# Kernel optimization log

Measured on AMD Instinct MI355X. Metric: run time of the kernel, lower is better.

The kernel has to match this reference:

```python
import jax, jax.numpy as jnp
import numpy as np

NUM_EMBEDDINGS = 1024
EMBEDDING_DIM = 512
SAMPLE_TOKENS = 4
CODE_DIM = EMBEDDING_DIM // SAMPLE_TOKENS  # 128
COMMITMENT_COST = 0.25


def setup_inputs() -> dict:
    key = jax.random.key(0)
    k1, k2 = jax.random.split(key)
    inputs = jax.random.normal(k1, (16, 1024, EMBEDDING_DIM), dtype=jnp.float32)
    # nn.Embedding weight init: uniform(-1/K, 1/K)
    emb_weight = jax.random.uniform(
        k2, (NUM_EMBEDDINGS, CODE_DIM), dtype=jnp.float32,
        minval=-1.0 / NUM_EMBEDDINGS, maxval=1.0 / NUM_EMBEDDINGS)
    return {"inputs": inputs, "emb_weight": emb_weight}


def reference(inputs, emb_weight):
    input_shape = inputs.shape
    flat = inputs.reshape(-1, CODE_DIM)  # [N, d]
    distances = (jnp.sum(flat * flat, axis=1, keepdims=True)
                 + jnp.sum(emb_weight * emb_weight, axis=1)
                 - 2.0 * jnp.matmul(flat, emb_weight.T))  # [N, K]
    encoding_indices = jnp.argmin(distances, axis=1)  # [N]
    # gather codebook rows instead of one-hot matmul (same math)
    quantized = jnp.take(emb_weight, encoding_indices, axis=0).reshape(input_shape)

    e_latent_loss = jnp.mean((jax.lax.stop_gradient(quantized) - inputs) ** 2)
    q_latent_loss = jnp.mean((quantized - jax.lax.stop_gradient(inputs)) ** 2)
    loss = q_latent_loss + COMMITMENT_COST * e_latent_loss

    # straight-through estimator
    quantized_ste = inputs + jax.lax.stop_gradient(quantized - inputs)

    # avg_probs = mean of one-hot encodings = code-usage histogram / N
    n = flat.shape[0]
    counts = jnp.zeros((NUM_EMBEDDINGS,), dtype=jnp.float32).at[encoding_indices].add(1.0)
    avg_probs = counts / n
    perplexity = jnp.exp(-jnp.sum(avg_probs * jnp.log(avg_probs + 1e-10)))

    return (quantized_ste, loss, perplexity)
```

## Files before the change

kernel.cpp:

```cpp
#include <hip/hip_runtime.h>
#include <cmath>

#define DIM      128
#define NELEMS   8388608
#define BAND_INT 12288
#define NBLOCKS  1024

typedef __attribute__((ext_vector_type(8))) short  short8;
typedef __attribute__((ext_vector_type(4))) float  f32x4;


__device__ inline unsigned short f2bf(float x) {
    unsigned u = __float_as_uint(x);
    unsigned r = u + 0x7FFFu + ((u >> 16) & 1u);
    return (unsigned short)(r >> 16);
}

__device__ __forceinline__ void gload_lds16(const void* g, void* l) {
    __builtin_amdgcn_global_load_lds(
        (const __attribute__((address_space(1))) void*)g,
        (__attribute__((address_space(3))) void*)l,
        16, 0, 0);
}

__global__ __launch_bounds__(256) void vq_prep_kernel(
        const float* __restrict__ e, unsigned short* __restrict__ Ehi,
        float* __restrict__ Bsq, int* __restrict__ counts, double* __restrict__ sse,
        int* __restrict__ done) {
    const int tid = threadIdx.x;
    {
        const int t  = blockIdx.x * 256 + tid;
        const int c  = t >> 4;
        const int gs = t & 15;
        const int kt = gs >> 2, qd = gs & 3;
        const int d0 = gs * 8;
        const float4 v0 = *(const float4*)(e + c * DIM + d0);
        const float4 v1 = *(const float4*)(e + c * DIM + d0 + 4);
        float f[8] = {v0.x, v0.y, v0.z, v0.w, v1.x, v1.y, v1.z, v1.w};
        unsigned short h[8];
        #pragma unroll
        for (int j = 0; j < 8; ++j) h[j] = f2bf(f[j]);
        const int ct = c >> 4, n = c & 15;
        uint4 ph;
        ph.x = h[0] | (h[1] << 16); ph.y = h[2] | (h[3] << 16);
        ph.z = h[4] | (h[5] << 16); ph.w = h[6] | (h[7] << 16);
        *(uint4*)&Ehi[(((ct * 4 + kt) * 64 + qd * 16 + n) * 8)] = ph;
    }
    {
        const int lane = tid & 31;
        #pragma unroll
        for (int r2 = 0; r2 < 2; ++r2) {
            const int row = blockIdx.x * 16 + (tid >> 5) * 2 + r2;
            const float4 xv = *(const float4*)(e + (size_t)row * DIM + lane * 4);
            float s = xv.x * xv.x + xv.y * xv.y + xv.z * xv.z + xv.w * xv.w;
            #pragma unroll
            for (int off = 16; off > 0; off >>= 1) s += __shfl_xor(s, off);
            if (lane == 0) Bsq[row] = s;
        }
    }
    if (blockIdx.x == 0) {
        ((int4*)counts)[tid] = make_int4(0, 0, 0, 0);
        if (tid == 0) { *sse = 0.0; *done = 0; }
    }
}

__global__ __launch_bounds__(256) void vq_main_kernel(
        const float* __restrict__ x, const float* __restrict__ emb,
        const unsigned short* __restrict__ Ehi, const float* __restrict__ Bsq,
        int* __restrict__ counts, double* __restrict__ sse,
        int* __restrict__ done, float* __restrict__ out) {
    __shared__ __align__(16) unsigned short Xs[8192];
    __shared__ float  sAsq[64];
    __shared__ int    sidx[64];
    __shared__ int    sIsLast;
    __shared__ double red[256];

    const int tid  = threadIdx.x;
    const int wave = tid >> 6;
    const int lane = tid & 63;
    const int n    = lane & 15;
    const int quad = lane >> 4;
    const int row0 = blockIdx.x * 64;

    {
        const int rl = tid >> 3, tq = tid & 7;
        const int dbase = tq * 16;
        const int rg_lo = rl >> 4, m = rl & 15;
        #pragma unroll
        for (int w = 0; w < 2; ++w) {
            const int r = 32 * w + rl;
            const float* xp = x + (size_t)(row0 + r) * DIM + dbase;
            float p[4];
            #pragma unroll
            for (int q = 0; q < 4; ++q) {
                const float4 v = *(const float4*)(xp + 4 * q);
                p[q] = v.x * v.x + v.y * v.y + v.z * v.z + v.w * v.w;
                const int dd = dbase + 4 * q;
                const int kt = dd >> 5, qd = (dd >> 3) & 3, j = dd & 7;
                unsigned short h0 = f2bf(v.x), h1 = f2bf(v.y), h2 = f2bf(v.z), h3 = f2bf(v.w);
                uint2 ph;
                ph.x = h0 | (h1 << 16); ph.y = h2 | (h3 << 16);
                const int rg = w * 2 + rg_lo;
                *(uint2*)&Xs[(((rg * 4 + kt) * 64 + qd * 16 + m) * 8) + j] = ph;
            }
            #pragma unroll
            for (int q = 0; q < 4; ++q) p[q] += __shfl_xor(p[q], 4);
            #pragma unroll
            for (int q = 0; q < 4; ++q) p[q] += __shfl_xor(p[q], 2);
            #pragma unroll
            for (int q = 0; q < 4; ++q) p[q] += __shfl_xor(p[q], 1);
            const float s = (p[0] + p[2]) + (p[1] + p[3]);
            if (tq == 0) sAsq[r] = s;
        }
    }
    __syncthreads();

    short8 Af[4];
    #pragma unroll
    for (int kt = 0; kt < 4; ++kt)
        Af[kt] = *(const short8*)&Xs[(((wave * 4 + kt) * 64 + lane) * 8)];
    __syncthreads();

    int K1[4], K2[4];
    #pragma unroll
    for (int i = 0; i < 4; ++i) { K1[i] = (int)0x80000000; K2[i] = (int)0x80000000; }

    const f32x4 cinit = {1.0f, 1.0f, 1.0f, 1.0f};

    #define STAGE(CUR, IT)                                                               \
        do {                                                                             \
            const char* _g = (const char*)Ehi + (size_t)(IT) * 8192 + wave * 2048 + lane * 16; \
            char*       _l = (char*)Xs + (CUR) * 8192 + wave * 2048;                     \
            gload_lds16(_g, _l);                                                         \
            gload_lds16(_g + 1024, _l + 1024);                                           \
        } while (0)

    int cur = 0;
    STAGE(0, 0);
    __syncthreads();
    for (int it = 0; it < 32; ++it) {
        if (it < 31) STAGE(cur ^ 1, it + 1);
        #pragma unroll
        for (int c = 0; c < 2; ++c) {
            const int ct = 2 * it + c;
            short8 Bf[4];
            #pragma unroll
            for (int kt = 0; kt < 4; ++kt)
                Bf[kt] = *(const short8*)&Xs[(size_t)cur * 4096 + c * 2048 + (kt * 64 + lane) * 8];
            f32x4 a = cinit;
            #pragma unroll
            for (int kt = 0; kt < 4; ++kt)
                a = __builtin_amdgcn_mfma_f32_16x16x32_bf16(Af[kt], Bf[kt], a, 0, 0, 0);
            #pragma unroll
            for (int r = 0; r < 4; ++r) {
                const int k0 = (__float_as_int(a[r]) & (int)0xFFFFFFC0) | ct;
                const int t0 = min(K1[r], k0);
                K1[r] = max(K1[r], k0);
                K2[r] = max(K2[r], t0);
            }
        }
        __syncthreads();
        cur ^= 1;
    }
    #undef STAGE

    int2* sc = (int2*)Xs;
    #pragma unroll
    for (int r = 0; r < 4; ++r) {
        const int lr = wave * 16 + quad * 4 + r;
        sc[lr * 17 + n] = make_int2(K1[r], K2[r]);
    }
    __syncthreads();

    if (tid < 64) {
        const int row  = tid;
        const int rowg = row0 + row;
        const int2* ent = (const int2*)sc + row * 17;
        int mx = (int)0x80000000;
        #pragma unroll
        for (int e2 = 0; e2 < 16; ++e2) mx = max(mx, ent[e2].x);
        const int thr = mx - BAND_INT;
        int ck[8];
        int nc = 0;
        #pragma unroll
        for (int e2 = 0; e2 < 16; ++e2) {
            const int2 kk = ent[e2];
            if (kk.x >= thr && nc < 8) ck[nc++] = ((kk.x & 63) << 4) | e2;
            if (kk.y >= thr && nc < 8) ck[nc++] = ((kk.y & 63) << 4) | e2;
        }
        float bd = INFINITY;
        int   bk = 0x7fffffff;
        const float4* xr = (const float4*)(x + (size_t)rowg * DIM);
        const float   aq = sAsq[row];
        for (int c = 0; c < nc; ++c) {
            const int k = ck[c];
            const float4* er = (const float4*)(emb + (size_t)k * DIM);
            float acc = 0.0f;
            #pragma unroll 4
            for (int dd = 0; dd < 32; ++dd) {
                const float4 xv = xr[dd];
                const float4 ev = er[dd];
                acc += xv.x * ev.x;
                acc += xv.y * ev.y;
                acc += xv.z * ev.z;
                acc += xv.w * ev.w;
            }
            const float t    = aq + Bsq[k];
            const float dist = t - 2.0f * acc;
            if (dist < bd || (dist == bd && k < bk)) { bd = dist; bk = k; }
        }
        sidx[row] = bk;
        atomicAdd(&counts[bk], 1);
        float ss = bd;
        #pragma unroll
        for (int off = 32; off > 0; off >>= 1) ss += __shfl_down(ss, off);
        if (tid == 0) atomicAdd(sse, (double)ss);
    }
    __syncthreads();

    #pragma unroll
    for (int i = tid; i < 2048; i += 256) {
        const int row = i >> 5, d4 = i & 31;
        const int k = sidx[row];
        const float4 xv = *((const float4*)(x + (size_t)(row0 + row) * DIM) + d4);
        const float4 qv = *((const float4*)emb + (size_t)k * 32 + d4);
        float4 ov;
        ov.x = xv.x + (qv.x - xv.x);
        ov.y = xv.y + (qv.y - xv.y);
        ov.z = xv.z + (qv.z - xv.z);
        ov.w = xv.w + (qv.w - xv.w);
        *((float4*)out + (size_t)(row0 + row) * 32 + d4) = ov;
    }

    if (tid == 0) sIsLast = (atomicAdd(done, 1) == NBLOCKS - 1);
    __syncthreads();
    if (sIsLast) {
        __threadfence();
        double s = 0.0;
        #pragma unroll
        for (int k = tid; k < 1024; k += 256) {
            const float p = (float)counts[k] * (1.0f / 65536.0f);
            s += (double)p * log((double)p + 1e-10);
        }
        red[tid] = s;
        __syncthreads();
        for (int st = 128; st > 0; st >>= 1) {
            if (tid < st) red[tid] += red[tid + st];
            __syncthreads();
        }
        if (tid == 0) {
            const float m = (float)(*sse * (1.0 / 8388608.0));
            out[NELEMS]     = m + 0.25f * m;
            out[NELEMS + 1] = (float)exp(-red[0]);
        }
    }
}

extern "C" void kernel_launch(void* const* d_in, const int* in_sizes, int n_in,
                              void* d_out, int out_size, void* d_ws, size_t ws_size,
                              hipStream_t stream) {
    const float* x   = (const float*)d_in[0];
    const float* emb = (const float*)d_in[1];
    float* out = (float*)d_out;

    char*           ws     = (char*)d_ws;
    float*          Bsq    = (float*)(ws + 0);
    int*            counts = (int*)(ws + 4096);
    double*         sse    = (double*)(ws + 8192);
    int*            done   = (int*)(ws + 12288);
    unsigned short* Ehi    = (unsigned short*)(ws + 16384);

    vq_prep_kernel<<<64, 256, 0, stream>>>(emb, Ehi, Bsq, counts, sse, done);
    vq_main_kernel<<<NBLOCKS, 256, 0, stream>>>(x, emb, Ehi, Bsq, counts, sse, done, out);
}
```

Before: 145.7 us.

## Split main kernel into scan and separate STE/finalize kernel

Moves the straight-through output write and the final loss/perplexity reduction out of the main kernel into a third launch. Nearest-code indices now go through a global buffer instead of shared memory. This drops the last-block done counter and its fence, which lets the scan kernel use fewer resources and run without a tail. In exchange it adds an extra launch and re-reads x from global memory, which is 32 MB of extra traffic.

Measured after the change: 152.7 us. 4.8% more time.

```diff
diff --git a/kernel.cpp b/kernel.cpp
--- a/kernel.cpp
+++ b/kernel.cpp
@@ -4,7 +4,6 @@
 #define DIM      128
 #define NELEMS   8388608
 #define BAND_INT 12288
-#define NBLOCKS  1024
 
 typedef __attribute__((ext_vector_type(8))) short  short8;
 typedef __attribute__((ext_vector_type(4))) float  f32x4;
@@ -25,8 +24,7 @@
 
 __global__ __launch_bounds__(256) void vq_prep_kernel(
         const float* __restrict__ e, unsigned short* __restrict__ Ehi,
-        float* __restrict__ Bsq, int* __restrict__ counts, double* __restrict__ sse,
-        int* __restrict__ done) {
+        float* __restrict__ Bsq, int* __restrict__ counts, double* __restrict__ sse) {
     const int tid = threadIdx.x;
     {
         const int t  = blockIdx.x * 256 + tid;
@@ -60,20 +58,17 @@
     }
     if (blockIdx.x == 0) {
         ((int4*)counts)[tid] = make_int4(0, 0, 0, 0);
-        if (tid == 0) { *sse = 0.0; *done = 0; }
-    }
-}
-
-__global__ __launch_bounds__(256) void vq_main_kernel(
+        if (tid == 0) *sse = 0.0;
+    }
+}
+
+__global__ __launch_bounds__(256) void vq_scan_kernel(
         const float* __restrict__ x, const float* __restrict__ emb,
         const unsigned short* __restrict__ Ehi, const float* __restrict__ Bsq,
         int* __restrict__ counts, double* __restrict__ sse,
-        int* __restrict__ done, float* __restrict__ out) {
+        int* __restrict__ sidx_g) {
     __shared__ __align__(16) unsigned short Xs[8192];
     __shared__ float  sAsq[64];
-    __shared__ int    sidx[64];
-    __shared__ int    sIsLast;
-    __shared__ double red[256];
 
     const int tid  = threadIdx.x;
     const int wave = tid >> 6;
@@ -209,50 +204,51 @@
             const float dist = t - 2.0f * acc;
             if (dist < bd || (dist == bd && k < bk)) { bd = dist; bk = k; }
         }
-        sidx[row] = bk;
+        sidx_g[rowg] = bk;
         atomicAdd(&counts[bk], 1);
         float ss = bd;
         #pragma unroll
         for (int off = 32; off > 0; off >>= 1) ss += __shfl_down(ss, off);
         if (tid == 0) atomicAdd(sse, (double)ss);
     }
-    __syncthreads();
-
-    #pragma unroll
-    for (int i = tid; i < 2048; i += 256) {
-        const int row = i >> 5, d4 = i & 31;
-        const int k = sidx[row];
-        const float4 xv = *((const float4*)(x + (size_t)(row0 + row) * DIM) + d4);
+}
+
+__global__ __launch_bounds__(256) void vq_ste_kernel(
+        const float* __restrict__ x, const float* __restrict__ emb,
+        const int* __restrict__ sidx, const int* __restrict__ counts,
+        const double* __restrict__ sse, float* __restrict__ out) {
+    const int tid = threadIdx.x;
+
+    if (blockIdx.x == 0 && tid < 64) {
+        double s = 0.0;
+        #pragma unroll
+        for (int k = tid; k < 1024; k += 64) {
+            const float p = (float)counts[k] * (1.0f / 65536.0f);
+            s += (double)p * log((double)p + 1e-10);
+        }
+        #pragma unroll
+        for (int off = 32; off > 0; off >>= 1) s += __shfl_down(s, off);
+        if (tid == 0) {
+            const float m = (float)(*sse * (1.0 / 8388608.0));
+            out[NELEMS]     = m + 0.25f * m;
+            out[NELEMS + 1] = (float)exp(-s);
+        }
+    }
+
+    const int total  = NELEMS / 4;
+    const int stride = gridDim.x * 256;
+    for (int i = blockIdx.x * 256 + tid; i < total; i += stride) {
+        const int row = i >> 5;
+        const int d4  = i & 31;
+        const int k   = sidx[row];
+        const float4 xv = *((const float4*)x + (size_t)row * 32 + d4);
         const float4 qv = *((const float4*)emb + (size_t)k * 32 + d4);
         float4 ov;
         ov.x = xv.x + (qv.x - xv.x);
         ov.y = xv.y + (qv.y - xv.y);
         ov.z = xv.z + (qv.z - xv.z);
         ov.w = xv.w + (qv.w - xv.w);
-        *((float4*)out + (size_t)(row0 + row) * 32 + d4) = ov;
-    }
-
-    if (tid == 0) sIsLast = (atomicAdd(done, 1) == NBLOCKS - 1);
-    __syncthreads();
-    if (sIsLast) {
-        __threadfence();
-        double s = 0.0;
-        #pragma unroll
-        for (int k = tid; k < 1024; k += 256) {
-            const float p = (float)counts[k] * (1.0f / 65536.0f);
-            s += (double)p * log((double)p + 1e-10);
-        }
-        red[tid] = s;
-        __syncthreads();
-        for (int st = 128; st > 0; st >>= 1) {
-            if (tid < st) red[tid] += red[tid + st];
-            __syncthreads();
-        }
-        if (tid == 0) {
-            const float m = (float)(*sse * (1.0 / 8388608.0));
-            out[NELEMS]     = m + 0.25f * m;
-            out[NELEMS + 1] = (float)exp(-red[0]);
-        }
+        *((float4*)out + i) = ov;
     }
 }
 
@@ -267,9 +263,10 @@
     float*          Bsq    = (float*)(ws + 0);
     int*            counts = (int*)(ws + 4096);
     double*         sse    = (double*)(ws + 8192);
-    int*            done   = (int*)(ws + 12288);
     unsigned short* Ehi    = (unsigned short*)(ws + 16384);
-
-    vq_prep_kernel<<<64, 256, 0, stream>>>(emb, Ehi, Bsq, counts, sse, done);
-    vq_main_kernel<<<NBLOCKS, 256, 0, stream>>>(x, emb, Ehi, Bsq, counts, sse, done, out);
-}
+    int*            sidx   = (int*)(ws + 278528);
+
+    vq_prep_kernel<<<64, 256, 0, stream>>>(emb, Ehi, Bsq, counts, sse);
+    vq_scan_kernel<<<1024, 256, 0, stream>>>(x, emb, Ehi, Bsq, counts, sse, sidx);
+    vq_ste_kernel<<<2048, 256, 0, stream>>>(x, emb, sidx, counts, sse, out);
+}
```

## Triple-buffer codebook staging and split waves into 2x2 row/column tiles

Applied to the files above, without the earlier changes.

Codebook tiles are now staged through three LDS buffers instead of two. Each iteration waits only for the older load with an explicit vmcnt wait and a raw s_barrier, so loads run two tiles ahead of compute. Waves are remapped so each owns two 16-row A tiles and one of the two 16-column B tiles per stage, which halves B-fragment LDS reads per MFMA and doubles the per-lane top-2 state. The candidate merge now scans 32 partial entries per row instead of 16. In exchange it uses more LDS and registers, and relies on hand-written wait counts being correct.

Result: slower. 174.3 us (+19.7%).

```diff
diff --git a/kernel.cpp b/kernel.cpp
--- a/kernel.cpp
+++ b/kernel.cpp
@@ -69,7 +69,7 @@
         const unsigned short* __restrict__ Ehi, const float* __restrict__ Bsq,
         int* __restrict__ counts, double* __restrict__ sse,
         int* __restrict__ done, float* __restrict__ out) {
-    __shared__ __align__(16) unsigned short Xs[8192];
+    __shared__ __align__(16) unsigned short Xs[12288];
     __shared__ float  sAsq[64];
     __shared__ int    sidx[64];
     __shared__ int    sIsLast;
@@ -80,6 +80,8 @@
     const int lane = tid & 63;
     const int n    = lane & 15;
     const int quad = lane >> 4;
+    const int wa   = wave >> 1;
+    const int ctb  = wave & 1;
     const int row0 = blockIdx.x * 64;
 
     {
@@ -115,78 +117,105 @@
     }
     __syncthreads();
 
-    short8 Af[4];
+    short8 Af[2][4];
     #pragma unroll
-    for (int kt = 0; kt < 4; ++kt)
-        Af[kt] = *(const short8*)&Xs[(((wave * 4 + kt) * 64 + lane) * 8)];
-    __syncthreads();
-
-    int K1[4], K2[4];
+    for (int rti = 0; rti < 2; ++rti)
+        #pragma unroll
+        for (int kt = 0; kt < 4; ++kt)
+            Af[rti][kt] = *(const short8*)&Xs[((((wa * 2 + rti) * 4 + kt) * 64 + lane) * 8)];
+    __syncthreads();
+
+    int K1[8], K2[8];
     #pragma unroll
-    for (int i = 0; i < 4; ++i) { K1[i] = (int)0x80000000; K2[i] = (int)0x80000000; }
+    for (int i = 0; i < 8; ++i) { K1[i] = (int)0x80000000; K2[i] = (int)0x80000000; }
 
     const f32x4 cinit = {1.0f, 1.0f, 1.0f, 1.0f};
 
-    #define STAGE(CUR, IT)                                                               \
+    #define STAGE(BUF, IT)                                                               \
         do {                                                                             \
             const char* _g = (const char*)Ehi + (size_t)(IT) * 8192 + wave * 2048 + lane * 16; \
-            char*       _l = (char*)Xs + (CUR) * 8192 + wave * 2048;                     \
+            char*       _l = (char*)Xs + (size_t)(BUF) * 8192 + wave * 2048;             \
             gload_lds16(_g, _l);                                                         \
             gload_lds16(_g + 1024, _l + 1024);                                           \
         } while (0)
 
-    int cur = 0;
+    #define COMPUTETILE(BUF, IT)                                                         \
+        do {                                                                             \
+            const int _ct = 2 * (IT) + ctb;                                              \
+            short8 Bf[4];                                                                \
+            _Pragma("unroll")                                                            \
+            for (int _kt = 0; _kt < 4; ++_kt)                                            \
+                Bf[_kt] = *(const short8*)&Xs[(size_t)(BUF) * 4096 + ctb * 2048 + (_kt * 64 + lane) * 8]; \
+            f32x4 _a0 = cinit, _a1 = cinit;                                              \
+            _Pragma("unroll")                                                            \
+            for (int _kt = 0; _kt < 4; ++_kt) {                                          \
+                _a0 = __builtin_amdgcn_mfma_f32_16x16x32_bf16(Af[0][_kt], Bf[_kt], _a0, 0, 0, 0); \
+                _a1 = __builtin_amdgcn_mfma_f32_16x16x32_bf16(Af[1][_kt], Bf[_kt], _a1, 0, 0, 0); \
+            }                                                                            \
+            _Pragma("unroll")                                                            \
+            for (int _r = 0; _r < 4; ++_r) {                                             \
+                int _k = (__float_as_int(_a0[_r]) & (int)0xFFFFFFC0) | _ct;              \
+                int _t = min(K1[_r], _k);                                                \
+                K1[_r] = max(K1[_r], _k);                                                \
+                K2[_r] = max(K2[_r], _t);                                                \
+                _k = (__float_as_int(_a1[_r]) & (int)0xFFFFFFC0) | _ct;                  \
+                _t = min(K1[4 + _r], _k);                                                \
+                K1[4 + _r] = max(K1[4 + _r], _k);                                        \
+                K2[4 + _r] = max(K2[4 + _r], _t);                                        \
+            }                                                                            \
+        } while (0)
+
+    int cur = 0, nxt = 1, fut = 2;
     STAGE(0, 0);
-    __syncthreads();
-    for (int it = 0; it < 32; ++it) {
-        if (it < 31) STAGE(cur ^ 1, it + 1);
-        #pragma unroll
-        for (int c = 0; c < 2; ++c) {
-            const int ct = 2 * it + c;
-            short8 Bf[4];
-            #pragma unroll
-            for (int kt = 0; kt < 4; ++kt)
-                Bf[kt] = *(const short8*)&Xs[(size_t)cur * 4096 + c * 2048 + (kt * 64 + lane) * 8];
-            f32x4 a = cinit;
-            #pragma unroll
-            for (int kt = 0; kt < 4; ++kt)
-                a = __builtin_amdgcn_mfma_f32_16x16x32_bf16(Af[kt], Bf[kt], a, 0, 0, 0);
-            #pragma unroll
-            for (int r = 0; r < 4; ++r) {
-                const int k0 = (__float_as_int(a[r]) & (int)0xFFFFFFC0) | ct;
-                const int t0 = min(K1[r], k0);
-                K1[r] = max(K1[r], k0);
-                K2[r] = max(K2[r], t0);
-            }
-        }
-        __syncthreads();
-        cur ^= 1;
-    }
+    STAGE(1, 1);
+    asm volatile("s_waitcnt vmcnt(2)" ::: "memory");
+    __builtin_amdgcn_sched_barrier(0);
+    __builtin_amdgcn_s_barrier();
+    __builtin_amdgcn_sched_barrier(0);
+
+    for (int it = 0; it < 30; ++it) {
+        STAGE(fut, it + 2);
+        COMPUTETILE(cur, it);
+        asm volatile("s_waitcnt vmcnt(2)" ::: "memory");
+        __builtin_amdgcn_sched_barrier(0);
+        __builtin_amdgcn_s_barrier();
+        __builtin_amdgcn_sched_barrier(0);
+        const int tmp = cur; cur = nxt; nxt = fut; fut = tmp;
+    }
+    COMPUTETILE(cur, 30);
+    __syncthreads();
+    { const int tmp = cur; cur = nxt; nxt = fut; fut = tmp; }
+    COMPUTETILE(cur, 31);
+    __syncthreads();
     #undef STAGE
+    #undef COMPUTETILE
 
     int2* sc = (int2*)Xs;
     #pragma unroll
-    for (int r = 0; r < 4; ++r) {
-        const int lr = wave * 16 + quad * 4 + r;
-        sc[lr * 17 + n] = make_int2(K1[r], K2[r]);
-    }
+    for (int rti = 0; rti < 2; ++rti)
+        #pragma unroll
+        for (int r = 0; r < 4; ++r) {
+            const int lr = (wa * 2 + rti) * 16 + quad * 4 + r;
+            sc[lr * 33 + ctb * 16 + n] = make_int2(K1[rti * 4 + r], K2[rti * 4 + r]);
+        }
     __syncthreads();
 
     if (tid < 64) {
         const int row  = tid;
         const int rowg = row0 + row;
-        const int2* ent = (const int2*)sc + row * 17;
+        const int2* ent = (const int2*)sc + row * 33;
         int mx = (int)0x80000000;
         #pragma unroll
-        for (int e2 = 0; e2 < 16; ++e2) mx = max(mx, ent[e2].x);
+        for (int e2 = 0; e2 < 32; ++e2) mx = max(mx, ent[e2].x);
         const int thr = mx - BAND_INT;
         int ck[8];
         int nc = 0;
         #pragma unroll
-        for (int e2 = 0; e2 < 16; ++e2) {
+        for (int e2 = 0; e2 < 32; ++e2) {
             const int2 kk = ent[e2];
-            if (kk.x >= thr && nc < 8) ck[nc++] = ((kk.x & 63) << 4) | e2;
-            if (kk.y >= thr && nc < 8) ck[nc++] = ((kk.y & 63) << 4) | e2;
+            const int ne = e2 & 15;
+            if (kk.x >= thr && nc < 8) ck[nc++] = ((kk.x & 63) << 4) | ne;
+            if (kk.y >= thr && nc < 8) ck[nc++] = ((kk.y & 63) << 4) | ne;
         }
         float bd = INFINITY;
         int   bk = 0x7fffffff;
```

## Use single-wave blocks over 32 rows with barrier-free double-buffered codebook streaming

Applied to the files above, without the earlier changes.

Each block becomes one 64-thread wave handling 32 rows (two MFMA row tiles that share each B fragment), and the grid doubles. Codebook tiles are loaded straight into LDS with an s_waitcnt-based two-deep pipeline instead of __syncthreads per iteration. The top-2 tracking uses v_med3, and the reductions switch to wave shuffles. The aim is to cut barrier overhead and reuse each B load across two row tiles. The cost is that each wave now streams the whole codebook into LDS by itself, with more LDS traffic per row, and correctness relies on the hand-written vmcnt counts.

After: 161.8 us. 11.1% more time.

```diff
diff --git a/kernel.cpp b/kernel.cpp
--- a/kernel.cpp
+++ b/kernel.cpp
@@ -4,7 +4,7 @@
 #define DIM      128
 #define NELEMS   8388608
 #define BAND_INT 12288
-#define NBLOCKS  1024
+#define NBLOCKS  2048
 
 typedef __attribute__((ext_vector_type(8))) short  short8;
 typedef __attribute__((ext_vector_type(4))) float  f32x4;
@@ -64,31 +64,29 @@
     }
 }
 
-__global__ __launch_bounds__(256) void vq_main_kernel(
+__global__ __launch_bounds__(64) void vq_main_kernel(
         const float* __restrict__ x, const float* __restrict__ emb,
         const unsigned short* __restrict__ Ehi, const float* __restrict__ Bsq,
         int* __restrict__ counts, double* __restrict__ sse,
         int* __restrict__ done, float* __restrict__ out) {
     __shared__ __align__(16) unsigned short Xs[8192];
-    __shared__ float  sAsq[64];
-    __shared__ int    sidx[64];
+    __shared__ float  sAsq[32];
+    __shared__ int    sidx[32];
     __shared__ int    sIsLast;
-    __shared__ double red[256];
 
     const int tid  = threadIdx.x;
-    const int wave = tid >> 6;
-    const int lane = tid & 63;
+    const int lane = tid;
     const int n    = lane & 15;
     const int quad = lane >> 4;
-    const int row0 = blockIdx.x * 64;
+    const int row0 = blockIdx.x * 32;
 
     {
         const int rl = tid >> 3, tq = tid & 7;
         const int dbase = tq * 16;
-        const int rg_lo = rl >> 4, m = rl & 15;
-        #pragma unroll
-        for (int w = 0; w < 2; ++w) {
-            const int r = 32 * w + rl;
+        #pragma unroll
+        for (int w = 0; w < 4; ++w) {
+            const int r = 8 * w + rl;
+            const int rg = r >> 4, m = r & 15;
             const float* xp = x + (size_t)(row0 + r) * DIM + dbase;
             float p[4];
             #pragma unroll
@@ -100,7 +98,6 @@
                 unsigned short h0 = f2bf(v.x), h1 = f2bf(v.y), h2 = f2bf(v.z), h3 = f2bf(v.w);
                 uint2 ph;
                 ph.x = h0 | (h1 << 16); ph.y = h2 | (h3 << 16);
-                const int rg = w * 2 + rg_lo;
                 *(uint2*)&Xs[(((rg * 4 + kt) * 64 + qd * 16 + m) * 8) + j] = ph;
             }
             #pragma unroll
@@ -115,64 +112,86 @@
     }
     __syncthreads();
 
-    short8 Af[4];
-    #pragma unroll
-    for (int kt = 0; kt < 4; ++kt)
-        Af[kt] = *(const short8*)&Xs[(((wave * 4 + kt) * 64 + lane) * 8)];
-    __syncthreads();
-
-    int K1[4], K2[4];
-    #pragma unroll
-    for (int i = 0; i < 4; ++i) { K1[i] = (int)0x80000000; K2[i] = (int)0x80000000; }
+    short8 Af[2][4];
+    #pragma unroll
+    for (int rti = 0; rti < 2; ++rti)
+        #pragma unroll
+        for (int kt = 0; kt < 4; ++kt)
+            Af[rti][kt] = *(const short8*)&Xs[(((rti * 4 + kt) * 64 + lane) * 8)];
+    __syncthreads();
+
+    int K1[8], K2[8];
+    #pragma unroll
+    for (int i = 0; i < 8; ++i) { K1[i] = (int)0x80000000; K2[i] = (int)0x80000000; }
 
     const f32x4 cinit = {1.0f, 1.0f, 1.0f, 1.0f};
 
-    #define STAGE(CUR, IT)                                                               \
-        do {                                                                             \
-            const char* _g = (const char*)Ehi + (size_t)(IT) * 8192 + wave * 2048 + lane * 16; \
-            char*       _l = (char*)Xs + (CUR) * 8192 + wave * 2048;                     \
-            gload_lds16(_g, _l);                                                         \
-            gload_lds16(_g + 1024, _l + 1024);                                           \
+    #define STAGE(BUF, IT)                                                         \
+        do {                                                                       \
+            const char* _g = (const char*)Ehi + (size_t)(IT) * 8192 + lane * 16;   \
+            char*       _l = (char*)Xs + (size_t)(BUF) * 8192 + lane * 16;         \
+            _Pragma("unroll")                                                      \
+            for (int _k = 0; _k < 8; ++_k)                                         \
+                gload_lds16(_g + _k * 1024, _l + _k * 1024);                       \
         } while (0)
 
-    int cur = 0;
+    #define COMPUTETILE(BUF, IT)                                                   \
+        do {                                                                       \
+            _Pragma("unroll")                                                      \
+            for (int _c = 0; _c < 2; ++_c) {                                       \
+                const int _ct = 2 * (IT) + _c;                                     \
+                short8 Bf[4];                                                      \
+                _Pragma("unroll")                                                  \
+                for (int _kt = 0; _kt < 4; ++_kt)                                  \
+                    Bf[_kt] = *(const short8*)&Xs[(size_t)(BUF) * 4096 + _c * 2048 + (_kt * 64 + lane) * 8]; \
+                f32x4 _a0 = cinit, _a1 = cinit;                                    \
+                _Pragma("unroll")                                                  \
+                for (int _kt = 0; _kt < 4; ++_kt) {                                \
+                    _a0 = __builtin_amdgcn_mfma_f32_16x16x32_bf16(Af[0][_kt], Bf[_kt], _a0, 0, 0, 0); \
+                    _a1 = __builtin_amdgcn_mfma_f32_16x16x32_bf16(Af[1][_kt], Bf[_kt], _a1, 0, 0, 0); \
+                }                                                                  \
+                _Pragma("unroll")                                                  \
+                for (int _r = 0; _r < 4; ++_r) {                                   \
+                    int _k0 = (__float_as_int(_a0[_r]) & (int)0xFFFFFFC0) | _ct;   \
+                    int _k2n;   \
+                    asm("v_med3_i32 %0, %1, %2, %3"                                \
+                        : "=v"(_k2n) : "v"(K1[_r]), "v"(K2[_r]), "v"(_k0));        \
+                    K2[_r] = _k2n;                                                 \
+                    K1[_r] = max(K1[_r], _k0);                                     \
+                    int _k1 = (__float_as_int(_a1[_r]) & (int)0xFFFFFFC0) | _ct;   \
+                    asm("v_med3_i32 %0, %1, %2, %3"                                \
+                        : "=v"(_k2n) : "v"(K1[4 + _r]), "v"(K2[4 + _r]), "v"(_k1)); \
+                    K2[4 + _r] = _k2n;                                             \
+                    K1[4 + _r] = max(K1[4 + _r], _k1);                             \
+                }                                                                  \
+            }                                                                      \
+        } while (0)
+
     STAGE(0, 0);
-    __syncthreads();
-    for (int it = 0; it < 32; ++it) {
-        if (it < 31) STAGE(cur ^ 1, it + 1);
-        #pragma unroll
-        for (int c = 0; c < 2; ++c) {
-            const int ct = 2 * it + c;
-            short8 Bf[4];
-            #pragma unroll
-            for (int kt = 0; kt < 4; ++kt)
-                Bf[kt] = *(const short8*)&Xs[(size_t)cur * 4096 + c * 2048 + (kt * 64 + lane) * 8];
-            f32x4 a = cinit;
-            #pragma unroll
-            for (int kt = 0; kt < 4; ++kt)
-                a = __builtin_amdgcn_mfma_f32_16x16x32_bf16(Af[kt], Bf[kt], a, 0, 0, 0);
-            #pragma unroll
-            for (int r = 0; r < 4; ++r) {
-                const int k0 = (__float_as_int(a[r]) & (int)0xFFFFFFC0) | ct;
-                const int t0 = min(K1[r], k0);
-                K1[r] = max(K1[r], k0);
-                K2[r] = max(K2[r], t0);
-            }
-        }
-        __syncthreads();
-        cur ^= 1;
-    }
+    STAGE(1, 1);
+    for (int it = 0; it < 31; ++it) {
+        asm volatile("s_waitcnt vmcnt(8)" ::: "memory");
+        COMPUTETILE(it & 1, it);
+        if (it < 30) STAGE(it & 1, it + 2);
+    }
+    asm volatile("s_waitcnt vmcnt(0)" ::: "memory");
+    COMPUTETILE(1, 31);
+    __syncthreads();
     #undef STAGE
+    #undef COMPUTETILE
 
     int2* sc = (int2*)Xs;
     #pragma unroll
-    for (int r = 0; r < 4; ++r) {
-        const int lr = wave * 16 + quad * 4 + r;
-        sc[lr * 17 + n] = make_int2(K1[r], K2[r]);
-    }
-    __syncthreads();
-
-    if (tid < 64) {
+    for (int rti = 0; rti < 2; ++rti)
+        #pragma unroll
+        for (int r = 0; r < 4; ++r) {
+            const int lr = rti * 16 + quad * 4 + r;
+            sc[lr * 17 + n] = make_int2(K1[rti * 4 + r], K2[rti * 4 + r]);
+        }
+    __syncthreads();
+
+    float ssum = 0.0f;
+    if (tid < 32) {
         const int row  = tid;
         const int rowg = row0 + row;
         const int2* ent = (const int2*)sc + row * 17;
@@ -211,15 +230,15 @@
         }
         sidx[row] = bk;
         atomicAdd(&counts[bk], 1);
-        float ss = bd;
-        #pragma unroll
-        for (int off = 32; off > 0; off >>= 1) ss += __shfl_down(ss, off);
-        if (tid == 0) atomicAdd(sse, (double)ss);
-    }
-    __syncthreads();
-
-    #pragma unroll
-    for (int i = tid; i < 2048; i += 256) {
+        ssum = bd;
+    }
+    #pragma unroll
+    for (int off = 32; off > 0; off >>= 1) ssum += __shfl_down(ssum, off);
+    if (tid == 0) atomicAdd(sse, (double)ssum);
+    __syncthreads();
+
+    #pragma unroll
+    for (int i = tid; i < 1024; i += 64) {
         const int row = i >> 5, d4 = i & 31;
         const int k = sidx[row];
         const float4 xv = *((const float4*)(x + (size_t)(row0 + row) * DIM) + d4);
@@ -238,20 +257,16 @@
         __threadfence();
         double s = 0.0;
         #pragma unroll
-        for (int k = tid; k < 1024; k += 256) {
+        for (int k = tid; k < 1024; k += 64) {
             const float p = (float)counts[k] * (1.0f / 65536.0f);
             s += (double)p * log((double)p + 1e-10);
         }
-        red[tid] = s;
-        __syncthreads();
-        for (int st = 128; st > 0; st >>= 1) {
-            if (tid < st) red[tid] += red[tid + st];
-            __syncthreads();
-        }
+        #pragma unroll
+        for (int off = 32; off > 0; off >>= 1) s += __shfl_down(s, off);
         if (tid == 0) {
             const float m = (float)(*sse * (1.0 / 8388608.0));
             out[NELEMS]     = m + 0.25f * m;
-            out[NELEMS + 1] = (float)exp(-red[0]);
+            out[NELEMS + 1] = (float)exp(-s);
         }
     }
 }
@@ -271,5 +286,5 @@
     unsigned short* Ehi    = (unsigned short*)(ws + 16384);
 
     vq_prep_kernel<<<64, 256, 0, stream>>>(emb, Ehi, Bsq, counts, sse, done);
-    vq_main_kernel<<<NBLOCKS, 256, 0, stream>>>(x, emb, Ehi, Bsq, counts, sse, done, out);
-}
+    vq_main_kernel<<<NBLOCKS, 64, 0, stream>>>(x, emb, Ehi, Bsq, counts, sse, done, out);
+}
```
